# Kernel optimization log

Hardware: AMD Instinct MI355X
Metric: run time of the kernel (lower is better)

Reference implementation:

```python
import jax, jax.numpy as jnp
import numpy as np

B, L, H, N = 4, 4096, 1024, 16
EPS = 1e-6  # layer_norm_epsilon


def setup_inputs() -> dict:
    key = jax.random.key(0)
    ks = jax.random.split(key, 8)
    hidden_states = jax.random.normal(ks[0], (B, L, H), dtype=jnp.float32)
    attention_mask = jnp.ones((B, L), dtype=jnp.float32)
    norm_weight = jnp.ones((H,), dtype=jnp.float32)
    # S4D init: dt log-uniform in [1e-3, 1e-1]; S4D-Lin A init; random C, D
    dt_min, dt_max = 1e-3, 1e-1
    log_dt = jax.random.uniform(ks[1], (H,), dtype=jnp.float32) * (
        float(np.log(dt_max)) - float(np.log(dt_min))) + float(np.log(dt_min))
    log_A_real = jnp.log(0.5 * jnp.ones((H, N), dtype=jnp.float32))
    A_imag = jnp.broadcast_to(float(np.pi) * jnp.arange(N, dtype=jnp.float32), (H, N))
    C_real = jax.random.normal(ks[2], (H, N), dtype=jnp.float32) * (0.5 ** 0.5)
    C_imag = jax.random.normal(ks[3], (H, N), dtype=jnp.float32) * (0.5 ** 0.5)
    D = jax.random.normal(ks[4], (H,), dtype=jnp.float32)
    out_w = jax.random.normal(ks[5], (2 * H, H), dtype=jnp.float32) * 0.02  # 1x1 conv to 2H (GLU)
    out_b = jnp.zeros((2 * H,), dtype=jnp.float32)
    return dict(hidden_states=hidden_states, attention_mask=attention_mask,
                norm_weight=norm_weight, log_dt=log_dt, log_A_real=log_A_real,
                A_imag=A_imag, C_real=C_real, C_imag=C_imag, D=D,
                out_w=out_w, out_b=out_b)


def _s4d_kernel(log_dt, log_A_real, A_imag, C_real, C_imag, length):
    """Diagonal SSM convolution kernel k[h, l] (S4D ZOH discretization)."""
    dt = jnp.exp(log_dt)                                   # (H,)
    A = -jnp.exp(log_A_real) + 1j * A_imag                 # (H, N) complex64
    C = C_real + 1j * C_imag                               # (H, N)
    dtA = A * dt[:, None]                                  # (H, N)
    C_disc = C * (jnp.exp(dtA) - 1.0) / A                  # (H, N)
    vand = jnp.exp(dtA[:, :, None] * jnp.arange(length, dtype=jnp.float32))  # (H, N, L)
    k = 2.0 * jnp.einsum('hn,hnl->hl', C_disc, vand).real  # (H, L)
    return k.astype(jnp.float32)


def reference(hidden_states, attention_mask, norm_weight, log_dt, log_A_real,
              A_imag, C_real, C_imag, D, out_w, out_b):
    # LongT5LayerNorm: RMSNorm (no mean subtraction), variance in fp32
    var = jnp.mean(jnp.square(hidden_states.astype(jnp.float32)), axis=-1, keepdims=True)
    normed = hidden_states * jax.lax.rsqrt(var + EPS) * norm_weight  # (B, L, H)
    # mask padded positions, go to channel-major layout (B, H, L)
    u = (normed * attention_mask[..., None]).transpose(0, 2, 1)
    Lx = u.shape[-1]
    k = _s4d_kernel(log_dt, log_A_real, A_imag, C_real, C_imag, Lx)  # (H, L)
    # causal convolution via FFT of length 2L
    nfft = 2 * Lx
    k_f = jnp.fft.rfft(k, n=nfft)                 # (H, nfft//2+1)
    u_f = jnp.fft.rfft(u, n=nfft)                 # (B, H, nfft//2+1)
    y = jnp.fft.irfft(u_f * k_f, n=nfft)[..., :Lx]  # (B, H, L)
    y = y + u * D[:, None]                        # skip connection
    y = jax.nn.gelu(y, approximate=False)         # torch nn.GELU (exact)
    # output 1x1 conv to 2H, then GLU over the channel dim
    z = jnp.einsum('bhl,oh->bol', y, out_w) + out_b[:, None]
    a, b = jnp.split(z, 2, axis=1)
    ssm_out = (a * jax.nn.sigmoid(b)).transpose(0, 2, 1)  # (B, L, H)
    # residual + dropout (eval mode -> identity)
    return hidden_states + ssm_out
```

## Files before the change

kernel.cpp:

```cpp
#include <hip/hip_runtime.h>

#define B_   4
#define L_   4096
#define H_   1024
#define N_   16
#define CH_  64
#define NC_  (L_/CH_)
#define M_   (B_*L_)
#define O2_  (2*H_)
#define EPS_ 1e-6f

typedef __attribute__((ext_vector_type(4))) float  f32x4;
typedef __attribute__((ext_vector_type(8))) __bf16 bf16x8;

__device__ __forceinline__ unsigned short f2bf(float x) {
  union { float f; unsigned int u; } v; v.f = x;
  unsigned int r = v.u + 0x7FFFu + ((v.u >> 16) & 1u);
  return (unsigned short)(r >> 16);
}
__device__ __forceinline__ float bf2f(unsigned short x) {
  union { unsigned int u; float f; } v; v.u = ((unsigned int)x) << 16;
  return v.f;
}

__device__ __forceinline__ void async_copy16(const void* g, void* l) {
  __builtin_amdgcn_global_load_lds(
      (const __attribute__((address_space(1))) unsigned int*)g,
      (__attribute__((address_space(3))) unsigned int*)l, 16, 0, 0);
}

__global__ void k_prep(const float* __restrict__ log_dt,
                       const float* __restrict__ log_A_real,
                       const float* __restrict__ A_imag,
                       const float* __restrict__ C_real,
                       const float* __restrict__ C_imag,
                       const float* __restrict__ outw,
                       const float* __restrict__ outb,
                       float* __restrict__ wr,  float* __restrict__ wi,
                       float* __restrict__ c2r, float* __restrict__ c2i,
                       float* __restrict__ wpr, float* __restrict__ wpi,
                       unsigned short* __restrict__ Wbf,
                       float* __restrict__ bp) {
  int idx = blockIdx.x * 256 + threadIdx.x;
  int p = idx >> 10, hh = idx & (H_ - 1);
  size_t src = (size_t)((p >> 1) + (p & 1) * H_) * H_ + hh;
  Wbf[idx] = f2bf(outw[src]);
  if (idx < O2_) bp[idx] = outb[(idx >> 1) + (idx & 1) * H_];
  if (idx < H_ * N_) {
    int h = idx / N_, n = idx % N_;
    int hn = h * N_ + n;
    float dt  = expf(log_dt[h]);
    float Ar  = -expf(log_A_real[hn]);
    float Ai  = A_imag[hn];
    float dr  = Ar * dt, di = Ai * dt;
    float er  = expf(dr);
    float wrv = er * cosf(di), wiv = er * sinf(di);
    float e1r = wrv - 1.0f, e1i = wiv;
    float den = Ar * Ar + Ai * Ai;
    float qr  = (e1r * Ar + e1i * Ai) / den;
    float qi  = (e1i * Ar - e1r * Ai) / den;
    float Cr  = C_real[hn], Ci = C_imag[hn];
    float cdr = Cr * qr - Ci * qi;
    float cdi = Cr * qi + Ci * qr;
    float ep  = expf((float)CH_ * dr);
    int o = n * H_ + h;
    wr[o]  = wrv;  wi[o]  = wiv;
    c2r[o] = 2.0f * cdr; c2i[o] = 2.0f * cdi;
    wpr[o] = ep * cosf((float)CH_ * di);
    wpi[o] = ep * sinf((float)CH_ * di);
  }
}

__global__ __launch_bounds__(256) void k_scale(const float* __restrict__ hs,
                                               const float* __restrict__ mask,
                                               float* __restrict__ scale) {
  int m = blockIdx.x, tid = threadIdx.x;
  float4 v = reinterpret_cast<const float4*>(hs + (size_t)m * H_)[tid];
  float s = v.x * v.x + v.y * v.y + v.z * v.z + v.w * v.w;
  #pragma unroll
  for (int off = 32; off > 0; off >>= 1) s += __shfl_down(s, off, 64);
  __shared__ float ps[4];
  if ((tid & 63) == 0) ps[tid >> 6] = s;
  __syncthreads();
  if (tid == 0) {
    float var = (ps[0] + ps[1] + ps[2] + ps[3]) * (1.0f / H_);
    scale[m] = rsqrtf(var + EPS_) * mask[m];
  }
}

__global__ __launch_bounds__(256) void k_scan1(const float* __restrict__ hs,
                                               const float* __restrict__ nw,
                                               const float* __restrict__ scale,
                                               const float* __restrict__ wr_,
                                               const float* __restrict__ wi_,
                                               float* __restrict__ endr,
                                               float* __restrict__ endi,
                                               unsigned short* __restrict__ ubf) {
  int tid = threadIdx.x;
  int h = blockIdx.x * 256 + tid;
  int c = blockIdx.y, b = blockIdx.z;
  float wr[N_], wi[N_], xr[N_], xi[N_];
  #pragma unroll
  for (int n = 0; n < N_; n++) {
    wr[n] = wr_[n * H_ + h]; wi[n] = wi_[n * H_ + h];
    xr[n] = 0.f; xi[n] = 0.f;
  }
  float nwh = nw[h];
  int l0 = c * CH_;
  const float* scp = scale + (size_t)b * L_ + l0;
  const float* hp = hs + ((size_t)b * L_ + l0) * H_ + h;
  unsigned short* up = ubf + ((size_t)b * L_ + l0) * H_ + h;
  #pragma unroll 8
  for (int l = 0; l < CH_; l++) {
    float u = hp[(size_t)l * H_] * scp[l] * nwh;
    unsigned short ub = f2bf(u);
    up[(size_t)l * H_] = ub;
    u = bf2f(ub);
    #pragma unroll
    for (int n = 0; n < N_; n++) {
      float oxr = xr[n];
      xr[n] = fmaf(wr[n], oxr, fmaf(-wi[n], xi[n], u));
      xi[n] = fmaf(wr[n], xi[n], wi[n] * oxr);
    }
  }
  size_t base = (((size_t)b * NC_ + c) * N_) * H_ + h;
  #pragma unroll
  for (int n = 0; n < N_; n++) {
    endr[base + (size_t)n * H_] = xr[n];
    endi[base + (size_t)n * H_] = xi[n];
  }
}

__global__ __launch_bounds__(256) void k_carry(const float* __restrict__ wpr_,
                                               const float* __restrict__ wpi_,
                                               const float* __restrict__ endr,
                                               const float* __restrict__ endi,
                                               float* __restrict__ carr,
                                               float* __restrict__ cari) {
  int idx = blockIdx.x * 256 + threadIdx.x;
  int h = idx & (H_ - 1);
  int n = (idx >> 10) & (N_ - 1);
  int b = idx >> 14;
  float wprv = wpr_[n * H_ + h], wpiv = wpi_[n * H_ + h];
  float sr = 0.f, si = 0.f;
  size_t cstride = (size_t)N_ * H_;
  size_t base = ((size_t)b * NC_) * cstride + (size_t)n * H_ + h;
  for (int c = 0; c < NC_; c++, base += cstride) {
    carr[base] = sr; cari[base] = si;
    float er = endr[base], ei = endi[base];
    float osr = sr;
    sr = fmaf(wprv, osr,  fmaf(-wpiv, si, er));
    si = fmaf(wprv, si, fmaf(wpiv, osr, ei));
  }
}

__global__ __launch_bounds__(256) void k_scan2(const unsigned short* __restrict__ ubf,
                                               const float* __restrict__ wr_,
                                               const float* __restrict__ wi_,
                                               const float* __restrict__ c2r_,
                                               const float* __restrict__ c2i_,
                                               const float* __restrict__ Dp,
                                               const float* __restrict__ carr,
                                               const float* __restrict__ cari,
                                               unsigned short* __restrict__ ybf) {
  int tid = threadIdx.x;
  int hb = blockIdx.x;
  int c = blockIdx.y, b = blockIdx.z;
  int h = hb * 256 + tid;
  int l0 = c * CH_;
  float wrv[N_], wiv[N_], crv[N_], civ[N_], xr[N_], xi[N_];
  size_t base = (((size_t)b * NC_ + c) * N_) * H_ + h;
  #pragma unroll
  for (int n = 0; n < N_; n++) {
    wrv[n] = wr_[n * H_ + h];  wiv[n] = wi_[n * H_ + h];
    crv[n] = c2r_[n * H_ + h]; civ[n] = c2i_[n * H_ + h];
    xr[n]  = carr[base + (size_t)n * H_];
    xi[n]  = cari[base + (size_t)n * H_];
  }
  float Dh = Dp[h];
  const unsigned short* up = ubf + ((size_t)b * L_ + l0) * H_ + h;
  unsigned short* yp = ybf + ((size_t)b * L_ + l0) * H_ + h;
  #pragma unroll 4
  for (int l = 0; l < CH_; l++) {
    float u = bf2f(up[(size_t)l * H_]);
    float y = Dh * u;
    #pragma unroll
    for (int n = 0; n < N_; n++) {
      float oxr = xr[n];
      xr[n] = fmaf(wrv[n], oxr, fmaf(-wiv[n], xi[n], u));
      xi[n] = fmaf(wrv[n], xi[n], wiv[n] * oxr);
      y = fmaf(crv[n], xr[n], fmaf(-civ[n], xi[n], y));
    }
    float g = 0.5f * y * (1.0f + erff(y * 0.70710678118654752f));
    yp[(size_t)l * H_] = f2bf(g);
  }
}

#define BM2 256
#define BN2 256
#define NT2 16
#define GST 132
#define GEMM_LDS 131072

#define STAGE_A(buf, half, kt) do { \
  async_copy16(Ag + (size_t)(bm + rp0 + ((half) << 6)) * H_ + (kt) * 64 + ca0, \
               sA + (buf) * 32768 + ((half) << 13) + tid * 16); \
  async_copy16(Ag + (size_t)(bm + rp1 + 64 + ((half) << 6)) * H_ + (kt) * 64 + ca1, \
               sA + (buf) * 32768 + ((half) << 13) + 16384 + tid * 16); \
} while (0)

#define STAGE_B(buf, eo, kt) do { \
  async_copy16(Bg + (size_t)(bn + ((rp0 >> 5) << 6) + (rp0 & 31) + ((eo) << 5)) * H_ + (kt) * 64 + ca0, \
               sB + (buf) * 32768 + ((rp0 >> 5) << 13) + ((rp0 & 31) << 7) + ((eo) << 12) + (q0 << 4)); \
  async_copy16(Bg + (size_t)(bn + ((rp1 >> 5) << 6) + (rp1 & 31) + ((eo) << 5)) * H_ + (kt) * 64 + ca1, \
               sB + (buf) * 32768 + ((rp1 >> 5) << 13) + ((rp1 & 31) << 7) + ((eo) << 12) + (q0 << 4)); \
} while (0)

#define VM4  asm volatile("s_waitcnt vmcnt(4)" ::: "memory")
#define NOVM do {} while (0)

#define LOAD_A(buf, mh) do { \
  _Pragma("unroll") \
  for (int m2 = 0; m2 < 4; m2++) { \
    _Pragma("unroll") \
    for (int kk = 0; kk < 2; kk++) \
      afr[m2][kk] = *reinterpret_cast<const bf16x8*>( \
          sA + (buf) * 32768 + (((wm << 7) + ((mh) << 6) + (m2 << 4)) << 7) + aoff[kk]); \
  } \
} while (0)

#define LOAD_B2(buf) do { \
  _Pragma("unroll") \
  for (int n2 = 0; n2 < 4; n2++) { \
    _Pragma("unroll") \
    for (int kk = 0; kk < 2; kk++) \
      bfr[n2][kk] = *reinterpret_cast<const bf16x8*>( \
          sB + (buf) * 32768 + (((wn << 6) + (n2 << 4)) << 7) + aoff[kk]); \
  } \
} while (0)

#define PH2(mh, LOADS, STAGE1, STAGE2, CLOSE_STMT) do { \
  LOADS; \
  STAGE1; \
  STAGE2; \
  asm volatile("" ::: "memory"); \
  __builtin_amdgcn_s_barrier(); \
  asm volatile("s_waitcnt lgkmcnt(0)" ::: "memory"); \
  __builtin_amdgcn_sched_barrier(0); \
  __builtin_amdgcn_s_setprio(1); \
  _Pragma("unroll") \
  for (int m2 = 0; m2 < 4; m2++) { \
    _Pragma("unroll") \
    for (int n2 = 0; n2 < 4; n2++) { \
      _Pragma("unroll") \
      for (int kk = 0; kk < 2; kk++) \
        acc[(mh) * 4 + m2][n2] = __builtin_amdgcn_mfma_f32_16x16x32_bf16( \
            afr[m2][kk], bfr[n2][kk], acc[(mh) * 4 + m2][n2], 0, 0, 0); \
    } \
  } \
  __builtin_amdgcn_s_setprio(0); \
  CLOSE_STMT; \
  asm volatile("" ::: "memory"); \
  __builtin_amdgcn_s_barrier(); \
  asm volatile("" ::: "memory"); \
} while (0)

__global__ __launch_bounds__(512, 2) void k_gemm(const unsigned short* __restrict__ Ag,
                                                 const unsigned short* __restrict__ Bg,
                                                 const float* __restrict__ bp,
                                                 const float* __restrict__ hs,
                                                 float* __restrict__ out) {
  extern __shared__ __align__(16) char smem[];
  char* sA = smem;
  char* sB = smem + 65536;
  const int tid  = threadIdx.x;
  const int lane = tid & 63;
  const int wave = tid >> 6;
  const int wm = wave >> 2;
  const int wn = wave & 3;
  const int lin = blockIdx.y * 8 + blockIdx.x;
  const int w   = ((lin & 7) << 6) + (lin >> 3);
  const int bn  = (w & 7) * BN2;
  const int bm  = (w >> 3) * BM2;
  const int ar = lane & 15, kqi = lane >> 4;

  const int rp0 = tid >> 3, q0 = tid & 7;
  const int rp1 = rp0 + 64;
  const int ca0 = (q0 ^ (rp0 & 7)) * 8;
  const int ca1 = (q0 ^ (rp1 & 7)) * 8;
  int aoff[2];
  #pragma unroll
  for (int kk = 0; kk < 2; kk++)
    aoff[kk] = ar * 128 + (((kk * 4 + kqi) ^ (ar & 7)) << 4);

  f32x4 acc[8][4];
  #pragma unroll
  for (int mi = 0; mi < 8; mi++)
    #pragma unroll
    for (int ni = 0; ni < 4; ni++) acc[mi][ni] = (f32x4){0.f, 0.f, 0.f, 0.f};

  bf16x8 afr[4][2], bfr[4][2];

  STAGE_A(0, 0, 0);
  STAGE_B(0, 0, 0);
  STAGE_A(0, 1, 0);
  STAGE_B(0, 1, 0);
  STAGE_A(1, 0, 1);
  STAGE_B(1, 1, 1);
  VM4;
  __builtin_amdgcn_s_barrier();
  asm volatile("" ::: "memory");

  #pragma unroll 1
  for (int i = 0; i < NT2 / 2; i++) {
    const int tb = 2 * i + 1;
    const int tc = (2 * i + 2 < NT2) ? 2 * i + 2 : NT2 - 1;
    const int td = (2 * i + 3 < NT2) ? 2 * i + 3 : NT2 - 1;
    PH2(0, LOAD_A(0, 0); LOAD_B2(0), STAGE_A(1, 1, tb), STAGE_B(1, 0, tb), NOVM);
    PH2(1, LOAD_A(0, 1),             STAGE_A(0, 0, tc), STAGE_B(0, 1, tc), VM4);
    PH2(0, LOAD_A(1, 0); LOAD_B2(1), STAGE_A(0, 1, tc), STAGE_B(0, 0, tc), NOVM);
    PH2(1, LOAD_A(1, 1),             STAGE_A(1, 0, td), STAGE_B(1, 1, td), VM4);
  }
  asm volatile("s_waitcnt vmcnt(0)" ::: "memory");
  __builtin_amdgcn_s_barrier();
  asm volatile("" ::: "memory");

  float* gt = (float*)smem;
  #pragma unroll
  for (int hf = 0; hf < 2; hf++) {
    if (wm == hf) {
      #pragma unroll
      for (int ni = 0; ni < 4; ni++) {
        int p  = wn * 64 + ni * 16 + (lane & 15);
        int pe = (bn + p) & ~1;
        float bA = bp[pe], bB = bp[pe + 1];
        int jl = p >> 1;
        #pragma unroll
        for (int mi = 0; mi < 8; mi++) {
          int lrow0 = mi * 16 + (lane >> 4) * 4;
          #pragma unroll
          for (int r = 0; r < 4; r++) {
            float v = acc[mi][ni][r];
            float w2 = __shfl_xor(v, 1, 64);
            if (!(lane & 1))
              gt[(lrow0 + r) * GST + jl] = (v + bA) / (1.0f + __expf(-(w2 + bB)));
          }
        }
      }
    }
    __syncthreads();
    {
      const int c4 = tid & 31;
      const int rw = tid >> 5;
      const size_t obase = (size_t)(bm + hf * 128) * H_ + (bn >> 1);
      #pragma unroll
      for (int rep = 0; rep < 8; rep++) {
        int row = rep * 16 + rw;
        float4 g = *reinterpret_cast<const float4*>(&gt[row * GST + c4 * 4]);
        size_t o = obase + (size_t)row * H_ + c4 * 4;
        float4 hv = *reinterpret_cast<const float4*>(&hs[o]);
        float4 rv = {hv.x + g.x, hv.y + g.y, hv.z + g.z, hv.w + g.w};
        *reinterpret_cast<float4*>(&out[o]) = rv;
      }
    }
    __syncthreads();
  }
}

extern "C" void kernel_launch(void* const* d_in, const int* in_sizes, int n_in,
                              void* d_out, int out_size, void* d_ws, size_t ws_size,
                              hipStream_t stream) {
  const float* hs    = (const float*)d_in[0];
  const float* mask  = (const float*)d_in[1];
  const float* nw    = (const float*)d_in[2];
  const float* ldt   = (const float*)d_in[3];
  const float* lar   = (const float*)d_in[4];
  const float* aim   = (const float*)d_in[5];
  const float* crl   = (const float*)d_in[6];
  const float* cim   = (const float*)d_in[7];
  const float* Dp    = (const float*)d_in[8];
  const float* outw  = (const float*)d_in[9];
  const float* outb  = (const float*)d_in[10];
  float* out = (float*)d_out;

  static bool attr_done = false;
  if (!attr_done) {
    hipFuncSetAttribute((const void*)k_gemm,
                        hipFuncAttributeMaxDynamicSharedMemorySize, GEMM_LDS);
    attr_done = true;
  }

  size_t off = 0;
  char* ws = (char*)d_ws;
  auto nxt = [&](size_t bytes) -> void* {
    void* p = ws + off; off += (bytes + 255) & ~(size_t)255; return p;
  };
  float* wr   = (float*)nxt(H_ * N_ * 4);
  float* wi   = (float*)nxt(H_ * N_ * 4);
  float* c2r  = (float*)nxt(H_ * N_ * 4);
  float* c2i  = (float*)nxt(H_ * N_ * 4);
  float* wpr  = (float*)nxt(H_ * N_ * 4);
  float* wpi  = (float*)nxt(H_ * N_ * 4);
  float* bpck = (float*)nxt(O2_ * 4);
  float* scale= (float*)nxt((size_t)M_ * 4);
  float* endr = (float*)nxt((size_t)B_ * NC_ * N_ * H_ * 4);
  float* endi = (float*)nxt((size_t)B_ * NC_ * N_ * H_ * 4);
  float* carr = (float*)nxt((size_t)B_ * NC_ * N_ * H_ * 4);
  float* cari = (float*)nxt((size_t)B_ * NC_ * N_ * H_ * 4);
  unsigned short* Wbf = (unsigned short*)nxt((size_t)O2_ * H_ * 2);
  unsigned short* ubf = (unsigned short*)nxt((size_t)M_ * H_ * 2);
  unsigned short* ybf = (unsigned short*)nxt((size_t)M_ * H_ * 2);

  k_prep<<<dim3(O2_ * H_ / 256), dim3(256), 0, stream>>>(ldt, lar, aim, crl, cim,
                                                         outw, outb,
                                                         wr, wi, c2r, c2i, wpr, wpi,
                                                         Wbf, bpck);
  k_scale<<<dim3(M_), dim3(256), 0, stream>>>(hs, mask, scale);
  k_scan1<<<dim3(H_ / 256, NC_, B_), dim3(256), 0, stream>>>(hs, nw, scale, wr, wi,
                                                             endr, endi, ubf);
  k_carry<<<dim3(B_ * N_ * H_ / 256), dim3(256), 0, stream>>>(wpr, wpi, endr, endi, carr, cari);
  k_scan2<<<dim3(H_ / 256, NC_, B_), dim3(256), 0, stream>>>(ubf, wr, wi, c2r, c2i,
                                                             Dp, carr, cari, ybf);
  k_gemm<<<dim3(O2_ / BN2, M_ / BM2), dim3(512), GEMM_LDS, stream>>>(ybf, Wbf, bpck, hs, out);
}
```

Baseline: 369.7 us.

## Replace four-phase ping-pong GEMM pipeline with simple double-buffered loop

Replaces the GEMM main loop's four-phase schedule with a plain double-buffered loop. The old schedule interleaved half-tile async stages with partial vmcnt waits and two barriers per phase. The new loop stages the whole next k-tile at once, runs two MFMA groups, then waits with vmcnt(0) and one barrier per k-tile. This cuts barrier count and simplifies the schedule, but it gives up the finer overlap: each iteration now waits for all of its global loads to finish before moving on.

Result: no change. 372.3 us (+0.7%).

```diff
diff --git a/kernel.cpp b/kernel.cpp
--- a/kernel.cpp
+++ b/kernel.cpp
@@ -216,9 +216,6 @@
                sB + (buf) * 32768 + ((rp1 >> 5) << 13) + ((rp1 & 31) << 7) + ((eo) << 12) + (q0 << 4)); \
 } while (0)
 
-#define VM4  asm volatile("s_waitcnt vmcnt(4)" ::: "memory")
-#define NOVM do {} while (0)
-
 #define LOAD_A(buf, mh) do { \
   _Pragma("unroll") \
   for (int m2 = 0; m2 < 4; m2++) { \
@@ -239,15 +236,7 @@
   } \
 } while (0)
 
-#define PH2(mh, LOADS, STAGE1, STAGE2, CLOSE_STMT) do { \
-  LOADS; \
-  STAGE1; \
-  STAGE2; \
-  asm volatile("" ::: "memory"); \
-  __builtin_amdgcn_s_barrier(); \
-  asm volatile("s_waitcnt lgkmcnt(0)" ::: "memory"); \
-  __builtin_amdgcn_sched_barrier(0); \
-  __builtin_amdgcn_s_setprio(1); \
+#define MFMA_G(mh) do { \
   _Pragma("unroll") \
   for (int m2 = 0; m2 < 4; m2++) { \
     _Pragma("unroll") \
@@ -258,11 +247,11 @@
             afr[m2][kk], bfr[n2][kk], acc[(mh) * 4 + m2][n2], 0, 0, 0); \
     } \
   } \
-  __builtin_amdgcn_s_setprio(0); \
-  CLOSE_STMT; \
-  asm volatile("" ::: "memory"); \
-  __builtin_amdgcn_s_barrier(); \
-  asm volatile("" ::: "memory"); \
+} while (0)
+
+#define LGKM0 do { \
+  asm volatile("s_waitcnt lgkmcnt(0)" ::: "memory"); \
+  __builtin_amdgcn_sched_barrier(0); \
 } while (0)
 
 __global__ __launch_bounds__(512, 2) void k_gemm(const unsigned short* __restrict__ Ag,
@@ -302,28 +291,37 @@
   bf16x8 afr[4][2], bfr[4][2];
 
   STAGE_A(0, 0, 0);
+  STAGE_A(0, 1, 0);
   STAGE_B(0, 0, 0);
-  STAGE_A(0, 1, 0);
   STAGE_B(0, 1, 0);
-  STAGE_A(1, 0, 1);
-  STAGE_B(1, 1, 1);
-  VM4;
-  __builtin_amdgcn_s_barrier();
-  asm volatile("" ::: "memory");
-
-  #pragma unroll 1
-  for (int i = 0; i < NT2 / 2; i++) {
-    const int tb = 2 * i + 1;
-    const int tc = (2 * i + 2 < NT2) ? 2 * i + 2 : NT2 - 1;
-    const int td = (2 * i + 3 < NT2) ? 2 * i + 3 : NT2 - 1;
-    PH2(0, LOAD_A(0, 0); LOAD_B2(0), STAGE_A(1, 1, tb), STAGE_B(1, 0, tb), NOVM);
-    PH2(1, LOAD_A(0, 1),             STAGE_A(0, 0, tc), STAGE_B(0, 1, tc), VM4);
-    PH2(0, LOAD_A(1, 0); LOAD_B2(1), STAGE_A(0, 1, tc), STAGE_B(0, 0, tc), NOVM);
-    PH2(1, LOAD_A(1, 1),             STAGE_A(1, 0, td), STAGE_B(1, 1, td), VM4);
-  }
   asm volatile("s_waitcnt vmcnt(0)" ::: "memory");
   __builtin_amdgcn_s_barrier();
   asm volatile("" ::: "memory");
+
+  #pragma unroll 1
+  for (int t = 0; t < NT2; t++) {
+    const int b = t & 1;
+    LOAD_A(b, 0);
+    LOAD_B2(b);
+    if (t + 1 < NT2) {
+      STAGE_A(b ^ 1, 0, t + 1);
+      STAGE_A(b ^ 1, 1, t + 1);
+      STAGE_B(b ^ 1, 0, t + 1);
+      STAGE_B(b ^ 1, 1, t + 1);
+    }
+    LGKM0;
+    __builtin_amdgcn_s_setprio(1);
+    MFMA_G(0);
+    __builtin_amdgcn_s_setprio(0);
+    LOAD_A(b, 1);
+    LGKM0;
+    __builtin_amdgcn_s_setprio(1);
+    MFMA_G(1);
+    __builtin_amdgcn_s_setprio(0);
+    asm volatile("s_waitcnt vmcnt(0)" ::: "memory");
+    __builtin_amdgcn_s_barrier();
+    asm volatile("" ::: "memory");
+  }
 
   float* gt = (float*)smem;
   #pragma unroll
```

## Restructure GEMM mainloop into 4-stage K=32 ring buffer with one barrier per tile

Applied to the files above, without the earlier changes.

Replaces the two-buffer, half-tile-phased K=64 mainloop with a four-slot ring of K=32 tiles. Each tile is staged three steps ahead, and there is one barrier per tile instead of two per half-tile. The LDS swizzle and fragment layout are simplified to single bf16x8 fragments per row group. This aims for deeper prefetch and fewer barriers, at the cost of twice as many iterations, each with less MFMA work to hide LDS-load latency.

Measured after the change: 377.7 us. 2.2% more time.

```diff
diff --git a/kernel.cpp b/kernel.cpp
--- a/kernel.cpp
+++ b/kernel.cpp
@@ -198,68 +198,57 @@
 
 #define BM2 256
 #define BN2 256
-#define NT2 16
+#define NT3 32
 #define GST 132
 #define GEMM_LDS 131072
 
-#define STAGE_A(buf, half, kt) do { \
-  async_copy16(Ag + (size_t)(bm + rp0 + ((half) << 6)) * H_ + (kt) * 64 + ca0, \
-               sA + (buf) * 32768 + ((half) << 13) + tid * 16); \
-  async_copy16(Ag + (size_t)(bm + rp1 + 64 + ((half) << 6)) * H_ + (kt) * 64 + ca1, \
-               sA + (buf) * 32768 + ((half) << 13) + 16384 + tid * 16); \
+#define SBUF(b) (smem + (size_t)(b) * 32768)
+
+#define STG(kt) do { \
+  char* dst = SBUF((kt) & 3); \
+  const unsigned short* as = Ag + (size_t)(bm + (tid >> 2)) * H_ + (kt) * 32 + scol; \
+  const unsigned short* bs = Bg + (size_t)(bn + (tid >> 2)) * H_ + (kt) * 32 + scol; \
+  async_copy16(as,                       dst + tid * 16); \
+  async_copy16(as + (size_t)128 * H_,    dst + 8192 + tid * 16); \
+  async_copy16(bs,                       dst + 16384 + tid * 16); \
+  async_copy16(bs + (size_t)128 * H_,    dst + 24576 + tid * 16); \
 } while (0)
 
-#define STAGE_B(buf, eo, kt) do { \
-  async_copy16(Bg + (size_t)(bn + ((rp0 >> 5) << 6) + (rp0 & 31) + ((eo) << 5)) * H_ + (kt) * 64 + ca0, \
-               sB + (buf) * 32768 + ((rp0 >> 5) << 13) + ((rp0 & 31) << 7) + ((eo) << 12) + (q0 << 4)); \
-  async_copy16(Bg + (size_t)(bn + ((rp1 >> 5) << 6) + (rp1 & 31) + ((eo) << 5)) * H_ + (kt) * 64 + ca1, \
-               sB + (buf) * 32768 + ((rp1 >> 5) << 13) + ((rp1 & 31) << 7) + ((eo) << 12) + (q0 << 4)); \
+#define LOADF3(buf) do { \
+  char* sb = SBUF(buf); \
+  _Pragma("unroll") \
+  for (int m2 = 0; m2 < 8; m2++) \
+    afr[m2] = *reinterpret_cast<const bf16x8*>(sb + (wm << 13) + (m2 << 10) + aoff3); \
+  _Pragma("unroll") \
+  for (int n2 = 0; n2 < 4; n2++) \
+    bfr[n2] = *reinterpret_cast<const bf16x8*>(sb + 16384 + (wn << 12) + (n2 << 10) + aoff3); \
 } while (0)
 
-#define VM4  asm volatile("s_waitcnt vmcnt(4)" ::: "memory")
-#define NOVM do {} while (0)
-
-#define LOAD_A(buf, mh) do { \
+#define MFMA3 do { \
   _Pragma("unroll") \
-  for (int m2 = 0; m2 < 4; m2++) { \
+  for (int m2 = 0; m2 < 8; m2++) { \
     _Pragma("unroll") \
-    for (int kk = 0; kk < 2; kk++) \
-      afr[m2][kk] = *reinterpret_cast<const bf16x8*>( \
-          sA + (buf) * 32768 + (((wm << 7) + ((mh) << 6) + (m2 << 4)) << 7) + aoff[kk]); \
+    for (int n2 = 0; n2 < 4; n2++) \
+      acc[m2][n2] = __builtin_amdgcn_mfma_f32_16x16x32_bf16( \
+          afr[m2], bfr[n2], acc[m2][n2], 0, 0, 0); \
   } \
 } while (0)
 
-#define LOAD_B2(buf) do { \
-  _Pragma("unroll") \
-  for (int n2 = 0; n2 < 4; n2++) { \
-    _Pragma("unroll") \
-    for (int kk = 0; kk < 2; kk++) \
-      bfr[n2][kk] = *reinterpret_cast<const bf16x8*>( \
-          sB + (buf) * 32768 + (((wn << 6) + (n2 << 4)) << 7) + aoff[kk]); \
-  } \
-} while (0)
-
-#define PH2(mh, LOADS, STAGE1, STAGE2, CLOSE_STMT) do { \
-  LOADS; \
-  STAGE1; \
-  STAGE2; \
+#define VM8 asm volatile("s_waitcnt vmcnt(8)" ::: "memory")
+#define VM4 asm volatile("s_waitcnt vmcnt(4)" ::: "memory")
+#define VM0 asm volatile("s_waitcnt vmcnt(0)" ::: "memory")
+#define NOP_ do {} while (0)
+
+#define TILE3(kt, DOSTAGE, VMWAIT) do { \
+  DOSTAGE; \
   asm volatile("" ::: "memory"); \
-  __builtin_amdgcn_s_barrier(); \
+  LOADF3((kt) & 3); \
   asm volatile("s_waitcnt lgkmcnt(0)" ::: "memory"); \
   __builtin_amdgcn_sched_barrier(0); \
   __builtin_amdgcn_s_setprio(1); \
-  _Pragma("unroll") \
-  for (int m2 = 0; m2 < 4; m2++) { \
-    _Pragma("unroll") \
-    for (int n2 = 0; n2 < 4; n2++) { \
-      _Pragma("unroll") \
-      for (int kk = 0; kk < 2; kk++) \
-        acc[(mh) * 4 + m2][n2] = __builtin_amdgcn_mfma_f32_16x16x32_bf16( \
-            afr[m2][kk], bfr[n2][kk], acc[(mh) * 4 + m2][n2], 0, 0, 0); \
-    } \
-  } \
+  MFMA3; \
   __builtin_amdgcn_s_setprio(0); \
-  CLOSE_STMT; \
+  VMWAIT; \
   asm volatile("" ::: "memory"); \
   __builtin_amdgcn_s_barrier(); \
   asm volatile("" ::: "memory"); \
@@ -271,8 +260,6 @@
                                                  const float* __restrict__ hs,
                                                  float* __restrict__ out) {
   extern __shared__ __align__(16) char smem[];
-  char* sA = smem;
-  char* sB = smem + 65536;
   const int tid  = threadIdx.x;
   const int lane = tid & 63;
   const int wave = tid >> 6;
@@ -282,16 +269,10 @@
   const int w   = ((lin & 7) << 6) + (lin >> 3);
   const int bn  = (w & 7) * BN2;
   const int bm  = (w >> 3) * BM2;
-  const int ar = lane & 15, kqi = lane >> 4;
-
-  const int rp0 = tid >> 3, q0 = tid & 7;
-  const int rp1 = rp0 + 64;
-  const int ca0 = (q0 ^ (rp0 & 7)) * 8;
-  const int ca1 = (q0 ^ (rp1 & 7)) * 8;
-  int aoff[2];
-  #pragma unroll
-  for (int kk = 0; kk < 2; kk++)
-    aoff[kk] = ar * 128 + (((kk * 4 + kqi) ^ (ar & 7)) << 4);
+  const int ar  = lane & 15, kg = lane >> 4;
+
+  const int scol = (((tid & 3) ^ ((tid >> 3) & 3)) << 3);
+  const int aoff3 = ar * 64 + (((kg ^ ((ar >> 1) & 3))) << 4);
 
   f32x4 acc[8][4];
   #pragma unroll
@@ -299,31 +280,22 @@
     #pragma unroll
     for (int ni = 0; ni < 4; ni++) acc[mi][ni] = (f32x4){0.f, 0.f, 0.f, 0.f};
 
-  bf16x8 afr[4][2], bfr[4][2];
-
-  STAGE_A(0, 0, 0);
-  STAGE_B(0, 0, 0);
-  STAGE_A(0, 1, 0);
-  STAGE_B(0, 1, 0);
-  STAGE_A(1, 0, 1);
-  STAGE_B(1, 1, 1);
-  VM4;
+  bf16x8 afr[8], bfr[4];
+
+  STG(0);
+  STG(1);
+  STG(2);
+  VM8;
   __builtin_amdgcn_s_barrier();
   asm volatile("" ::: "memory");
 
   #pragma unroll 1
-  for (int i = 0; i < NT2 / 2; i++) {
-    const int tb = 2 * i + 1;
-    const int tc = (2 * i + 2 < NT2) ? 2 * i + 2 : NT2 - 1;
-    const int td = (2 * i + 3 < NT2) ? 2 * i + 3 : NT2 - 1;
-    PH2(0, LOAD_A(0, 0); LOAD_B2(0), STAGE_A(1, 1, tb), STAGE_B(1, 0, tb), NOVM);
-    PH2(1, LOAD_A(0, 1),             STAGE_A(0, 0, tc), STAGE_B(0, 1, tc), VM4);
-    PH2(0, LOAD_A(1, 0); LOAD_B2(1), STAGE_A(0, 1, tc), STAGE_B(0, 0, tc), NOVM);
-    PH2(1, LOAD_A(1, 1),             STAGE_A(1, 0, td), STAGE_B(1, 1, td), VM4);
-  }
-  asm volatile("s_waitcnt vmcnt(0)" ::: "memory");
-  __builtin_amdgcn_s_barrier();
-  asm volatile("" ::: "memory");
+  for (int t = 0; t < NT3 - 3; t++) {
+    TILE3(t, STG(t + 3), VM8);
+  }
+  TILE3(NT3 - 3, NOP_, VM4);
+  TILE3(NT3 - 2, NOP_, VM0);
+  TILE3(NT3 - 1, NOP_, NOP_);
 
   float* gt = (float*)smem;
   #pragma unroll
```
